# Optimization experiments

Measured on AMD Instinct MI355X. Metric: run time of the kernel, lower is better.

## Reference

```python
import jax, jax.numpy as jnp
import numpy as np


def setup_inputs() -> dict:
    key = jax.random.key(0)
    k1, k2 = jax.random.split(key)
    N, C, H, W = 4, 128, 160, 320
    left = jax.random.normal(k1, (N, C, H, W), dtype=jnp.float32)
    right = jax.random.normal(k2, (N, C, H, W), dtype=jnp.float32)
    return {"left": left, "right": right, "max_disparity": 48}


def reference(left, right, max_disparity):
    # left, right: (N, C, H, W) -> volume: (N, D, H, W)
    # volume[n, d, h, w] = sum_c left[n, c, h, w] * right[n, c, h, w - d]  (0 if w < d)
    n, c, h, w = left.shape
    slices = []
    for d in range(max_disparity):  # fixed structural constant, unrolled at trace time
        # channel dot-product of overlapping strips, shape (N, H, W - d)
        corr = jnp.einsum('nchw,nchw->nhw', left[:, :, :, d:], right[:, :, :, :w - d])
        # left-pad the first d columns with zeros to restore width W
        slices.append(jnp.pad(corr, ((0, 0), (0, 0), (d, 0))))
    return jnp.stack(slices, axis=1)  # (N, D, H, W)
```

## Files before the change

kernel.cpp:

```cpp
#include <hip/hip_runtime.h>


#define NN 4
#define CC 128
#define HH 160
#define WW 320
#define DD 48
#define HWs (HH * WW)
#define NTH 256
#define GRID 3200

typedef _Float16 h2 __attribute__((ext_vector_type(2)));
typedef _Float16 f16x8 __attribute__((ext_vector_type(8)));
typedef float f32x4 __attribute__((ext_vector_type(4)));
typedef __fp16 h2raw __attribute__((ext_vector_type(2)));

__device__ __forceinline__ h2 pack2(float a, float b) {
  union { h2raw r; h2 h; } u;
  u.r = __builtin_amdgcn_cvt_pkrtz(a, b);
  return u.h;
}

__global__ __launch_bounds__(NTH, 4)
void corr_kernel(const float* __restrict__ L, const float* __restrict__ R,
                 float* __restrict__ out) {
  __shared__ __align__(16) float Ep[4][DD * 20];

  const int tid = threadIdx.x;
  const int wid = tid >> 6;
  const int ln  = tid & 63;
  const int i16 = ln & 15;
  const int g   = ln >> 4;

  const int hwb = blockIdx.x;
  const int bid = (hwb & 7) * (GRID / 8) + (hwb >> 3);

  const int row = bid / 5;
  const int grp = bid - 5 * row;
  const int n = row / HH;
  const int h = row - n * HH;
  const int w0 = 64 * grp + 16 * wid;

  const size_t base = (size_t)n * CC * HWs + (size_t)h * WW;
  const float* Lp = L + base + w0 + i16;
  const float* Rp = R + base + i16;

  union AU { f16x8 v; h2 h[4]; };

  float la[32];
#pragma unroll
  for (int ks = 0; ks < 4; ++ks)
#pragma unroll
    for (int e = 0; e < 8; ++e)
      la[ks * 8 + e] = Lp[(size_t)(32 * ks + 8 * g + e) * HWs];
  AU A[4];
#pragma unroll
  for (int ks = 0; ks < 4; ++ks)
#pragma unroll
    for (int j = 0; j < 4; ++j)
      A[ks].h[j] = pack2(la[ks * 8 + 2 * j], la[ks * 8 + 2 * j + 1]);

  f32x4 acc[4];
#pragma unroll
  for (int q = 0; q < 4; ++q) acc[q] = (f32x4){0.f, 0.f, 0.f, 0.f};

#pragma unroll
  for (int q = 0; q < 4; ++q) {
    const int j0 = w0 - 48 + 16 * q;
    const bool ok = (j0 >= 0);
    const float* rp = Rp + (ok ? j0 : 0);
    float rb[32];
#pragma unroll
    for (int ks = 0; ks < 4; ++ks)
#pragma unroll
      for (int e = 0; e < 8; ++e)
        rb[ks * 8 + e] = rp[(size_t)(32 * ks + 8 * g + e) * HWs];
    const h2 z = pack2(0.f, 0.f);
#pragma unroll
    for (int ks = 0; ks < 4; ++ks) {
      AU B;
#pragma unroll
      for (int j = 0; j < 4; ++j)
        B.h[j] = ok ? pack2(rb[ks * 8 + 2 * j], rb[ks * 8 + 2 * j + 1]) : z;
      acc[q] = __builtin_amdgcn_mfma_f32_16x16x32_f16(A[ks].v, B.v, acc[q], 0, 0, 0);
    }
  }

  float* ep = Ep[wid];
#pragma unroll
  for (int q = 0; q < 4; ++q)
#pragma unroll
    for (int r = 0; r < 4; ++r) {
      int d = 48 - 16 * q + 4 * g + r - i16;
      if (d >= 0 && d < DD) ep[d * 20 + 4 * g + r] = acc[q][r];
    }

  const int l4 = ln & 3;
  const int dr = ln >> 2;
  float* op = out + (size_t)n * DD * HWs + (size_t)h * WW + w0 + 4 * l4;
#pragma unroll
  for (int rr = 0; rr < 3; ++rr) {
    int d = 16 * rr + dr;
    *(float4*)&op[(size_t)d * HWs] = *(const float4*)&ep[d * 20 + 4 * l4];
  }
}

extern "C" void kernel_launch(void* const* d_in, const int* in_sizes, int n_in,
                              void* d_out, int out_size, void* d_ws, size_t ws_size,
                              hipStream_t stream) {
  const float* L = (const float*)d_in[0];
  const float* R = (const float*)d_in[1];
  float* out = (float*)d_out;
  corr_kernel<<<dim3(GRID), dim3(NTH), 0, stream>>>(L, R, out);
}
```

Before: 287.1 us.

## Stage shared right strips in LDS via async global_load_lds with double buffering

```diff
diff --git a/kernel.cpp b/kernel.cpp
--- a/kernel.cpp
+++ b/kernel.cpp
@@ -1,4 +1,5 @@
 #include <hip/hip_runtime.h>
+#include <stdint.h>
 
 
 #define NN 4
@@ -7,8 +8,12 @@
 #define WW 320
 #define DD 48
 #define HWs (HH * WW)
-#define NTH 256
-#define GRID 3200
+#define WB 160
+#define RJ 208
+#define CK 32
+#define CHF (CK * RJ)
+#define NTH 640
+#define GRID 1280
 
 typedef _Float16 h2 __attribute__((ext_vector_type(2)));
 typedef _Float16 f16x8 __attribute__((ext_vector_type(8)));
@@ -21,86 +26,109 @@
   return u.h;
 }
 
-__global__ __launch_bounds__(NTH, 4)
+__device__ __forceinline__ void gl_lds16(const float* g, float* l) {
+  __builtin_amdgcn_global_load_lds(
+      (const __attribute__((address_space(1))) uint32_t*)g,
+      (__attribute__((address_space(3))) uint32_t*)l, 16, 0, 0);
+}
+
+__global__ __launch_bounds__(NTH, 8)
 void corr_kernel(const float* __restrict__ L, const float* __restrict__ R,
                  float* __restrict__ out) {
-  __shared__ __align__(16) float Ep[4][DD * 20];
+  __shared__ __align__(16) float S[2 * CHF];
 
   const int tid = threadIdx.x;
-  const int wid = tid >> 6;
+  const int wt  = tid >> 6;
   const int ln  = tid & 63;
   const int i16 = ln & 15;
   const int g   = ln >> 4;
 
-  const int hwb = blockIdx.x;
-  const int bid = (hwb & 7) * (GRID / 8) + (hwb >> 3);
-
-  const int row = bid / 5;
-  const int grp = bid - 5 * row;
-  const int n = row / HH;
-  const int h = row - n * HH;
-  const int w0 = 64 * grp + 16 * wid;
+  const int raw = blockIdx.x;
+  const int bid = (raw & 7) * (GRID / 8) + (raw >> 3);
+  const int wsplit = bid & 1;
+  const int rnh = bid >> 1;
+  const int n = rnh / HH;
+  const int h = rnh - n * HH;
+  const int wb = wsplit * WB;
 
   const size_t base = (size_t)n * CC * HWs + (size_t)h * WW;
-  const float* Lp = L + base + w0 + i16;
-  const float* Rp = R + base + i16;
+  const float* Rb = R + base;
+  const float* Lb = L + base + wb + 16 * wt + i16;
 
-  union AU { f16x8 v; h2 h[4]; };
+  const int t0 = tid, t1 = tid + 640, t2 = tid + 1280;
+  const int c0 = t0 / 52, v0 = t0 - 52 * c0;
+  const int c1 = t1 / 52, v1 = t1 - 52 * c1;
+  const int c2 = t2 / 52, v2 = t2 - 52 * c2;
+  int col0 = wb - 48 + 4 * v0; if (col0 < 0) col0 = 0;
+  int col1 = wb - 48 + 4 * v1; if (col1 < 0) col1 = 0;
+  int col2 = wb - 48 + 4 * v2; if (col2 < 0) col2 = 0;
+  const float* gp0 = Rb + (size_t)c0 * HWs + col0;
+  const float* gp1 = Rb + (size_t)c1 * HWs + col1;
+  const float* gp2 = Rb + (size_t)c2 * HWs + col2;
 
-  float la[32];
-#pragma unroll
-  for (int ks = 0; ks < 4; ++ks)
+  float lv[2][8];
+
+  auto stage = [&](int kk) {
+    float* dst = S + (kk & 1) * CHF;
+    const size_t coff = (size_t)(CK * kk) * HWs;
+    gl_lds16(gp0 + coff, dst + 4 * t0);
+    gl_lds16(gp1 + coff, dst + 4 * t1);
+    if (wt < 6) gl_lds16(gp2 + coff, dst + 4 * t2);
+  };
+  auto lload = [&](int kk) {
+    const float* p = Lb + (size_t)(CK * kk) * HWs;
 #pragma unroll
     for (int e = 0; e < 8; ++e)
-      la[ks * 8 + e] = Lp[(size_t)(32 * ks + 8 * g + e) * HWs];
-  AU A[4];
-#pragma unroll
-  for (int ks = 0; ks < 4; ++ks)
-#pragma unroll
-    for (int j = 0; j < 4; ++j)
-      A[ks].h[j] = pack2(la[ks * 8 + 2 * j], la[ks * 8 + 2 * j + 1]);
+      lv[kk & 1][e] = p[(size_t)(4 * e + g) * HWs];
+  };
+
+  stage(0);
+  lload(0);
+  __syncthreads();
 
   f32x4 acc[4];
 #pragma unroll
   for (int q = 0; q < 4; ++q) acc[q] = (f32x4){0.f, 0.f, 0.f, 0.f};
 
 #pragma unroll
-  for (int q = 0; q < 4; ++q) {
-    const int j0 = w0 - 48 + 16 * q;
-    const bool ok = (j0 >= 0);
-    const float* rp = Rp + (ok ? j0 : 0);
-    float rb[32];
+  for (int k = 0; k < 4; ++k) {
+    if (k < 3) { stage(k + 1); lload(k + 1); }
+
+    union AU { f16x8 v; h2 h[4]; } A;
 #pragma unroll
-    for (int ks = 0; ks < 4; ++ks)
+    for (int j = 0; j < 4; ++j)
+      A.h[j] = pack2(lv[k & 1][2 * j], lv[k & 1][2 * j + 1]);
+
+    const float* Bb = S + (k & 1) * CHF;
 #pragma unroll
-      for (int e = 0; e < 8; ++e)
-        rb[ks * 8 + e] = rp[(size_t)(32 * ks + 8 * g + e) * HWs];
-    const h2 z = pack2(0.f, 0.f);
-#pragma unroll
-    for (int ks = 0; ks < 4; ++ks) {
-      AU B;
+    for (int q = 0; q < 4; ++q) {
+      const int s = 16 * (wt + q) + i16;
+      union BU { f16x8 v; h2 h[4]; } B;
 #pragma unroll
       for (int j = 0; j < 4; ++j)
-        B.h[j] = ok ? pack2(rb[ks * 8 + 2 * j], rb[ks * 8 + 2 * j + 1]) : z;
-      acc[q] = __builtin_amdgcn_mfma_f32_16x16x32_f16(A[ks].v, B.v, acc[q], 0, 0, 0);
+        B.h[j] = pack2(Bb[(8 * j + g) * RJ + s], Bb[(8 * j + 4 + g) * RJ + s]);
+      acc[q] = __builtin_amdgcn_mfma_f32_16x16x32_f16(A.v, B.v, acc[q], 0, 0, 0);
     }
+    __syncthreads();
   }
 
-  float* ep = Ep[wid];
+  float* ep = S + wt * (DD * 20);
+  const int wl = wb + 16 * wt;
 #pragma unroll
   for (int q = 0; q < 4; ++q)
 #pragma unroll
     for (int r = 0; r < 4; ++r) {
-      int d = 48 - 16 * q + 4 * g + r - i16;
-      if (d >= 0 && d < DD) ep[d * 20 + 4 * g + r] = acc[q][r];
+      const int m = 4 * g + r;
+      const int d = 48 - 16 * q + m - i16;
+      if (d >= 0 && d < DD) ep[d * 20 + m] = (d <= wl + m) ? acc[q][r] : 0.f;
     }
 
   const int l4 = ln & 3;
   const int dr = ln >> 2;
-  float* op = out + (size_t)n * DD * HWs + (size_t)h * WW + w0 + 4 * l4;
+  float* op = out + (size_t)n * DD * HWs + (size_t)h * WW + wl + 4 * l4;
 #pragma unroll
   for (int rr = 0; rr < 3; ++rr) {
-    int d = 16 * rr + dr;
+    const int d = 16 * rr + dr;
     *(float4*)&op[(size_t)d * HWs] = *(const float4*)&ep[d * 20 + 4 * l4];
   }
 }
```

Result: faster. 245.1 us (-14.6%).
